# Kernel optimization log

Measured on AMD Instinct MI355X. Metric: run time of the kernel, lower is better.

## Reference

```python
import jax, jax.numpy as jnp
import numpy as np

N = 100000
E = 3200000
F_IN = 512
HID = 8
NC = 64


def setup_inputs() -> dict:
    key = jax.random.key(0)
    ks = jax.random.split(key, 12)
    x = jax.random.normal(ks[0], (N, F_IN), dtype=jnp.float32)
    edge_index = jax.random.randint(ks[1], (2, E), 0, N, dtype=jnp.int64)
    # layer 1: lin(512 -> 8), wmlp: Linear(1,8,no bias) -> LeakyReLU(0.2) -> Linear(8,8,bias)
    W1 = jax.random.normal(ks[2], (F_IN, HID), dtype=jnp.float32) / np.sqrt(F_IN)
    b1 = jnp.zeros((HID,), dtype=jnp.float32)
    mW1a = jax.random.normal(ks[3], (1, HID), dtype=jnp.float32)
    mW1b = jax.random.normal(ks[4], (HID, HID), dtype=jnp.float32) / np.sqrt(HID)
    mb1 = jnp.zeros((HID,), dtype=jnp.float32)
    # layer 2: lin(8 -> 64), wmlp: Linear(1,64,no bias) -> LeakyReLU(0.2) -> Linear(64,64,bias)
    W2 = jax.random.normal(ks[5], (HID, NC), dtype=jnp.float32) / np.sqrt(HID)
    b2 = jnp.zeros((NC,), dtype=jnp.float32)
    mW2a = jax.random.normal(ks[6], (1, NC), dtype=jnp.float32)
    mW2b = jax.random.normal(ks[7], (NC, NC), dtype=jnp.float32) / np.sqrt(NC)
    mb2 = jnp.zeros((NC,), dtype=jnp.float32)
    return {"x": x, "edge_index": edge_index,
            "W1": W1, "b1": b1, "mW1a": mW1a, "mW1b": mW1b, "mb1": mb1,
            "W2": W2, "b2": b2, "mW2a": mW2a, "mW2b": mW2b, "mb2": mb2}


def _rcgn(x, edge_index, W, b, mWa, mWb, mb):
    n = x.shape[0]
    h = x @ W + b                                   # [N, C]
    row, col = edge_index[0], edge_index[1]
    # degree of source nodes only (matches degree(row, ...))
    deg = jax.ops.segment_sum(jnp.ones_like(row, dtype=h.dtype), row, num_segments=n)
    dinv = jnp.where(deg > 0, deg ** -0.5, 0.0)     # guard isolated nodes
    norm = (dinv[row] * dinv[col])[:, None]          # [E, 1]
    # per-edge MLP on scalar norm -> per-edge per-channel weight [E, C]
    w = jax.nn.leaky_relu(norm @ mWa, 0.2) @ mWb + mb
    msg = w * h[row]                                 # gather + elementwise [E, C]
    return jax.ops.segment_sum(msg, col, num_segments=n)  # scatter-add to targets


def reference(x, edge_index, W1, b1, mW1a, mW1b, mb1, W2, b2, mW2a, mW2b, mb2):
    # eval mode: dropout layers are identity
    h = _rcgn(x, edge_index, W1, b1, mW1a, mW1b, mb1)
    h = jax.nn.elu(h)
    h = _rcgn(h, edge_index, W2, b2, mW2a, mW2b, mb2)
    return jax.nn.log_softmax(h, axis=1)
```

## Files before the change

### kernel.cpp

```cpp
#include <hip/hip_runtime.h>
#include <hip/hip_bf16.h>
#include <math.h>

#define NNODES 100000
#define NEDGES 3200000
#define FIN 512
#define HID 8
#define NC 64

#define OFF_DEG      0u
#define OFF_CNT      1600000u
#define OFF_DINV     3200000u
#define OFF_COLPTR   3600000u
#define OFF_BSUM     4000004u
#define OFF_BOFF     4000516u
#define OFF_A1       4001028u
#define OFF_A2       4001060u
#define OFF_AUX      4001316u
#define OFF_CSR      7201320u
#define OFF_H1       0u
#define OFF_H2       32801320u

__global__ __launch_bounds__(256) void k_count(const int* __restrict__ ei,
                                               int* __restrict__ deg, int* __restrict__ cnt,
                                               unsigned char* __restrict__ aux) {
    int t = blockIdx.x * blockDim.x + threadIdx.x;
    if (t < NEDGES) {
        atomicAdd(&deg[ei[t] << 2], 1);
        int rank = atomicAdd(&cnt[ei[NEDGES + t] << 2], 1);
        aux[t] = (unsigned char)rank;
    }
}

__global__ __launch_bounds__(1024) void k_scan1(const int* __restrict__ cnt,
                                                const int* __restrict__ deg,
                                                float* __restrict__ dinv,
                                                int* __restrict__ colptr, int* __restrict__ bsum) {
    __shared__ int s[1024];
    int t = threadIdx.x, b = blockIdx.x;
    int i = b * 1024 + t;
    int v = (i < NNODES) ? cnt[i << 2] : 0;
    if (i < NNODES) {
        int d = deg[i << 2];
        dinv[i] = (d > 0) ? 1.0f / sqrtf((float)d) : 0.0f;
    }
    s[t] = v; __syncthreads();
    for (int off = 1; off < 1024; off <<= 1) {
        int add = (t >= off) ? s[t - off] : 0;
        __syncthreads();
        s[t] += add;
        __syncthreads();
    }
    if (i < NNODES) colptr[i + 1] = s[t];
    if (t == 1023) bsum[b] = s[1023];
}

__global__ __launch_bounds__(128) void k_scan2(const int* __restrict__ bsum,
                                               int* __restrict__ boff, int nb) {
    __shared__ int s[128];
    int t = threadIdx.x;
    int v = (t < nb) ? bsum[t] : 0;
    s[t] = v; __syncthreads();
    for (int off = 1; off < 128; off <<= 1) {
        int add = (t >= off) ? s[t - off] : 0;
        __syncthreads();
        s[t] += add;
        __syncthreads();
    }
    if (t < nb) boff[t] = s[t] - v;
}

__global__ __launch_bounds__(1024) void k_scan3(int* __restrict__ colptr, const int* __restrict__ boff) {
    int i = blockIdx.x * blockDim.x + threadIdx.x;
    if (i < NNODES) colptr[i + 1] += boff[i >> 10];
    if (i == 0) colptr[0] = 0;
}

__global__ __launch_bounds__(64) void k_precomp(const float* __restrict__ mW1a, const float* __restrict__ mW1b,
                                                const float* __restrict__ mW2a, const float* __restrict__ mW2b,
                                                float* __restrict__ A1, float* __restrict__ A2) {
    int t = threadIdx.x;
    if (t < 8) {
        float s = 0.f;
        for (int j = 0; j < 8; j++) {
            float a = mW1a[j]; a = a > 0.f ? a : 0.2f * a;
            s += a * mW1b[j * 8 + t];
        }
        A1[t] = s;
    }
    if (t < 64) {
        float s = 0.f;
        for (int j = 0; j < 64; j++) {
            float a = mW2a[j]; a = a > 0.f ? a : 0.2f * a;
            s += a * mW2b[j * 64 + t];
        }
        A2[t] = s;
    }
}

__global__ __launch_bounds__(256) void k_fill(const int* __restrict__ ei, const float* __restrict__ dinv,
                                              const int* __restrict__ colptr,
                                              const unsigned char* __restrict__ aux,
                                              int2* __restrict__ csr) {
    int t = blockIdx.x * blockDim.x + threadIdx.x;
    if (t < NEDGES) {
        int r = ei[t], c = ei[NEDGES + t];
        float nm = dinv[r] * dinv[c];
        int pos = colptr[c] + (int)aux[t];
        csr[pos] = make_int2(r, __float_as_int(nm));
    }
}

__global__ __launch_bounds__(256) void k_gemm1(const float* __restrict__ x, const float* __restrict__ W1,
                                               const float* __restrict__ b1, float* __restrict__ h1) {
    __shared__ float w[HID * FIN];
    for (int idx = threadIdx.x; idx < HID * FIN; idx += 256) {
        int j = idx >> 3, k = idx & 7;
        w[k * FIN + j] = W1[idx];
    }
    __syncthreads();
    int lane = threadIdx.x & 63;
    int node = blockIdx.x * 4 + (threadIdx.x >> 6);
    const float* xr = x + (size_t)node * FIN;
    float acc[8] = {0.f,0.f,0.f,0.f,0.f,0.f,0.f,0.f};
#pragma unroll
    for (int tt = 0; tt < 8; tt++) {
        float xv = xr[lane + 64 * tt];
#pragma unroll
        for (int k = 0; k < 8; k++)
            acc[k] += xv * w[k * FIN + lane + 64 * tt];
    }
    {
        bool hi = (lane & 32) != 0;
#pragma unroll
        for (int m = 0; m < 4; m++) {
            float send = hi ? acc[m] : acc[m + 4];
            float recv = __shfl_xor(send, 32, 64);
            acc[m] = (hi ? acc[m + 4] : acc[m]) + recv;
        }
    }
    {
        bool hi = (lane & 16) != 0;
#pragma unroll
        for (int m = 0; m < 2; m++) {
            float send = hi ? acc[m] : acc[m + 2];
            float recv = __shfl_xor(send, 16, 64);
            acc[m] = (hi ? acc[m + 2] : acc[m]) + recv;
        }
    }
    {
        bool hi = (lane & 8) != 0;
        float send = hi ? acc[0] : acc[1];
        float recv = __shfl_xor(send, 8, 64);
        acc[0] = (hi ? acc[1] : acc[0]) + recv;
    }
    acc[0] += __shfl_xor(acc[0], 4, 64);
    acc[0] += __shfl_xor(acc[0], 2, 64);
    acc[0] += __shfl_xor(acc[0], 1, 64);
    if ((lane & 7) == 0) {
        int k = (lane >> 3) & 7;
        h1[(size_t)node * HID + k] = acc[0] + b1[k];
    }
}

__global__ __launch_bounds__(256) void k_agg1(const int* __restrict__ colptr, const int2* __restrict__ csr,
                                              const float* __restrict__ h1, const float* __restrict__ A1,
                                              const float* __restrict__ mb1, const float* __restrict__ W2,
                                              const float* __restrict__ b2, float* __restrict__ h2) {
    int lane = threadIdx.x & 63;
    int node = blockIdx.x * 4 + (threadIdx.x >> 6);
    int k = lane & 7, esub = lane >> 3;
    float a1 = A1[k], m1 = mb1[k];
    int s = colptr[node], e = colptr[node + 1];
    float acc = 0.f;
    for (int i = s + esub; i < e; i += 8) {
        int2 ed = csr[i];
        float nm = __int_as_float(ed.y);
        acc += (nm * a1 + m1) * h1[(size_t)ed.x * HID + k];
    }
    acc += __shfl_xor(acc, 8, 64);
    acc += __shfl_xor(acc, 16, 64);
    acc += __shfl_xor(acc, 32, 64);
    float hv = acc > 0.f ? acc : expm1f(acc);
    float o = b2[lane];
#pragma unroll
    for (int j = 0; j < 8; j++) {
        float ev = __shfl(hv, j, 64);
        o += ev * W2[j * NC + lane];
    }
    h2[(size_t)node * NC + lane] = o;
}

__global__ __launch_bounds__(256) void k_agg2(const int* __restrict__ colptr, const int2* __restrict__ csr,
                                              const float* __restrict__ h2, const float* __restrict__ A2,
                                              const float* __restrict__ mb2, float* __restrict__ out) {
    int lane = threadIdx.x & 63;
    int node = blockIdx.x * 4 + (threadIdx.x >> 6);
    float a2 = A2[lane], m2 = mb2[lane];
    int s = colptr[node], e = colptr[node + 1];
    float acc = 0.f;
    int i = s;
    for (; i + 4 <= e; i += 4) {
        int2 e0 = csr[i], e1 = csr[i + 1], e2 = csr[i + 2], e3 = csr[i + 3];
        float h0 = h2[(size_t)e0.x * NC + lane];
        float h1v = h2[(size_t)e1.x * NC + lane];
        float h2v = h2[(size_t)e2.x * NC + lane];
        float h3 = h2[(size_t)e3.x * NC + lane];
        acc += (__int_as_float(e0.y) * a2 + m2) * h0;
        acc += (__int_as_float(e1.y) * a2 + m2) * h1v;
        acc += (__int_as_float(e2.y) * a2 + m2) * h2v;
        acc += (__int_as_float(e3.y) * a2 + m2) * h3;
    }
    for (; i < e; i++) {
        int2 ed = csr[i];
        acc += (__int_as_float(ed.y) * a2 + m2) * h2[(size_t)ed.x * NC + lane];
    }
    float m = acc;
#pragma unroll
    for (int o = 32; o >= 1; o >>= 1) m = fmaxf(m, __shfl_xor(m, o, 64));
    float ex = expf(acc - m);
    float ssum = ex;
#pragma unroll
    for (int o = 32; o >= 1; o >>= 1) ssum += __shfl_xor(ssum, o, 64);
    out[(size_t)node * NC + lane] = (acc - m) - logf(ssum);
}

extern "C" void kernel_launch(void* const* d_in, const int* in_sizes, int n_in,
                              void* d_out, int out_size, void* d_ws, size_t ws_size,
                              hipStream_t stream) {
    const float* x    = (const float*)d_in[0];
    const int*   ei   = (const int*)d_in[1];
    const float* W1   = (const float*)d_in[2];
    const float* b1   = (const float*)d_in[3];
    const float* mW1a = (const float*)d_in[4];
    const float* mW1b = (const float*)d_in[5];
    const float* mb1  = (const float*)d_in[6];
    const float* W2   = (const float*)d_in[7];
    const float* b2   = (const float*)d_in[8];
    const float* mW2a = (const float*)d_in[9];
    const float* mW2b = (const float*)d_in[10];
    const float* mb2  = (const float*)d_in[11];

    char* ws = (char*)d_ws;
    int*   deg    = (int*)(ws + OFF_DEG);
    int*   cnt    = (int*)(ws + OFF_CNT);
    float* dinv   = (float*)(ws + OFF_DINV);
    int*   colptr = (int*)(ws + OFF_COLPTR);
    int*   bsum   = (int*)(ws + OFF_BSUM);
    int*   boff   = (int*)(ws + OFF_BOFF);
    float* A1     = (float*)(ws + OFF_A1);
    float* A2     = (float*)(ws + OFF_A2);
    unsigned char* aux = (unsigned char*)(ws + OFF_AUX);
    int2*  csr    = (int2*)(ws + OFF_CSR);
    float* h1     = (float*)(ws + OFF_H1);
    float* h2     = (float*)(ws + OFF_H2);
    float* outp   = (float*)d_out;

    hipMemsetAsync(ws, 0, 3200000, stream);

    const int EB = (NEDGES + 255) / 256;
    const int SB = (NNODES + 1023) / 1024;

    k_count  <<<EB, 256, 0, stream>>>(ei, deg, cnt, aux);
    k_scan1  <<<SB, 1024, 0, stream>>>(cnt, deg, dinv, colptr, bsum);
    k_scan2  <<<1, 128, 0, stream>>>(bsum, boff, SB);
    k_scan3  <<<SB, 1024, 0, stream>>>(colptr, boff);
    k_precomp<<<1, 64, 0, stream>>>(mW1a, mW1b, mW2a, mW2b, A1, A2);
    k_fill   <<<EB, 256, 0, stream>>>(ei, dinv, colptr, aux, csr);
    k_gemm1  <<<NNODES / 4, 256, 0, stream>>>(x, W1, b1, h1);
    k_agg1   <<<NNODES / 4, 256, 0, stream>>>(colptr, csr, h1, A1, mb1, W2, b2, h2);
    k_agg2   <<<NNODES / 4, 256, 0, stream>>>(colptr, csr, h2, A2, mb2, outp);
}
```

Measured before the change: 880.1 us.

## Compute source degrees via LDS-privatized range histograms; register-resident W1 in gemm1

Replaces the global atomic degree count with a two-pass scheme. Blocks build shared-memory histograms over node-range/edge-chunk tiles into a slab, then a reduce kernel sums the slabs and writes dinv. The target-count atomics drop their 4x padding stride, and the workspace layout and memset shrink. The first GEMM now loads W1 rows into registers with float4 loads and reads x as float4 instead of staging W1 transposed in shared memory. The histogram pass reads the row array 8 times, and each thread now holds 64 weight registers.

```diff
diff --git a/kernel.cpp b/kernel.cpp
--- a/kernel.cpp
+++ b/kernel.cpp
@@ -8,42 +8,67 @@
 #define HID 8
 #define NC 64
 
-#define OFF_DEG      0u
-#define OFF_CNT      1600000u
-#define OFF_DINV     3200000u
-#define OFF_COLPTR   3600000u
-#define OFF_BSUM     4000004u
-#define OFF_BOFF     4000516u
-#define OFF_A1       4001028u
-#define OFF_A2       4001060u
-#define OFF_AUX      4001316u
-#define OFF_CSR      7201320u
-#define OFF_H1       0u
-#define OFF_H2       32801320u
+#define NRANGE 8
+#define NCHUNK 32
+#define ECHUNK (NEDGES / NCHUNK)
+#define RBINS  12500
+#define RPAD   12512
+
+#define OFF_CNT      0u
+#define OFF_DINV     400000u
+#define OFF_COLPTR   800000u
+#define OFF_BSUM     1200004u
+#define OFF_BOFF     1200516u
+#define OFF_A1       1201028u
+#define OFF_A2       1201060u
+#define OFF_AUX      1201316u
+#define OFF_H1       1201316u
+#define OFF_CSR      4401320u
+#define OFF_H2       30001320u
+
+__global__ __launch_bounds__(1024) void k_hist(const int* __restrict__ ei, int* __restrict__ slab) {
+    __shared__ int lh[RBINS];
+    int ri = blockIdx.x & 7, ci = blockIdx.x >> 3;
+    for (int b = threadIdx.x; b < RBINS; b += 1024) lh[b] = 0;
+    __syncthreads();
+    int base = ri * RBINS;
+    const int* rows = ei + (size_t)ci * ECHUNK;
+    for (int t = threadIdx.x; t < ECHUNK; t += 1024) {
+        int r = rows[t] - base;
+        if ((unsigned)r < RBINS) atomicAdd(&lh[r], 1);
+    }
+    __syncthreads();
+    int* out = slab + (size_t)blockIdx.x * RPAD;
+    for (int b = threadIdx.x; b < RBINS; b += 1024) out[b] = lh[b];
+}
+
+__global__ __launch_bounds__(256) void k_reduce(const int* __restrict__ slab, float* __restrict__ dinv) {
+    int i = blockIdx.x * 256 + threadIdx.x;
+    if (i >= NNODES) return;
+    int ri = i / RBINS, b = i - ri * RBINS;
+    int s = 0;
+#pragma unroll 4
+    for (int ci = 0; ci < NCHUNK; ci++)
+        s += slab[(size_t)(ci * NRANGE + ri) * RPAD + b];
+    dinv[i] = (s > 0) ? 1.0f / sqrtf((float)s) : 0.0f;
+}
 
 __global__ __launch_bounds__(256) void k_count(const int* __restrict__ ei,
-                                               int* __restrict__ deg, int* __restrict__ cnt,
+                                               int* __restrict__ cnt,
                                                unsigned char* __restrict__ aux) {
     int t = blockIdx.x * blockDim.x + threadIdx.x;
     if (t < NEDGES) {
-        atomicAdd(&deg[ei[t] << 2], 1);
-        int rank = atomicAdd(&cnt[ei[NEDGES + t] << 2], 1);
+        int rank = atomicAdd(&cnt[ei[NEDGES + t]], 1);
         aux[t] = (unsigned char)rank;
     }
 }
 
 __global__ __launch_bounds__(1024) void k_scan1(const int* __restrict__ cnt,
-                                                const int* __restrict__ deg,
-                                                float* __restrict__ dinv,
                                                 int* __restrict__ colptr, int* __restrict__ bsum) {
     __shared__ int s[1024];
     int t = threadIdx.x, b = blockIdx.x;
     int i = b * 1024 + t;
-    int v = (i < NNODES) ? cnt[i << 2] : 0;
-    if (i < NNODES) {
-        int d = deg[i << 2];
-        dinv[i] = (d > 0) ? 1.0f / sqrtf((float)d) : 0.0f;
-    }
+    int v = (i < NNODES) ? cnt[i] : 0;
     s[t] = v; __syncthreads();
     for (int off = 1; off < 1024; off <<= 1) {
         int add = (t >= off) ? s[t - off] : 0;
@@ -113,22 +138,32 @@
 
 __global__ __launch_bounds__(256) void k_gemm1(const float* __restrict__ x, const float* __restrict__ W1,
                                                const float* __restrict__ b1, float* __restrict__ h1) {
-    __shared__ float w[HID * FIN];
-    for (int idx = threadIdx.x; idx < HID * FIN; idx += 256) {
-        int j = idx >> 3, k = idx & 7;
-        w[k * FIN + j] = W1[idx];
-    }
-    __syncthreads();
     int lane = threadIdx.x & 63;
     int node = blockIdx.x * 4 + (threadIdx.x >> 6);
-    const float* xr = x + (size_t)node * FIN;
+    float w[8][8];
+#pragma unroll
+    for (int tf = 0; tf < 2; tf++) {
+        int jf = lane + 64 * tf;
+#pragma unroll
+        for (int m = 0; m < 4; m++) {
+            const float4* Wr = (const float4*)(W1 + (size_t)(4 * jf + m) * 8);
+            float4 lo = Wr[0], hi = Wr[1];
+            int r = 4 * tf + m;
+            w[r][0] = lo.x; w[r][1] = lo.y; w[r][2] = lo.z; w[r][3] = lo.w;
+            w[r][4] = hi.x; w[r][5] = hi.y; w[r][6] = hi.z; w[r][7] = hi.w;
+        }
+    }
+    const float4* xr = (const float4*)(x + (size_t)node * FIN);
     float acc[8] = {0.f,0.f,0.f,0.f,0.f,0.f,0.f,0.f};
 #pragma unroll
-    for (int tt = 0; tt < 8; tt++) {
-        float xv = xr[lane + 64 * tt];
-#pragma unroll
-        for (int k = 0; k < 8; k++)
-            acc[k] += xv * w[k * FIN + lane + 64 * tt];
+    for (int tf = 0; tf < 2; tf++) {
+        float4 xv = xr[lane + 64 * tf];
+        float xs[4] = {xv.x, xv.y, xv.z, xv.w};
+#pragma unroll
+        for (int m = 0; m < 4; m++)
+#pragma unroll
+            for (int k = 0; k < 8; k++)
+                acc[k] += xs[m] * w[4 * tf + m][k];
     }
     {
         bool hi = (lane & 32) != 0;
@@ -242,7 +277,6 @@
     const float* mb2  = (const float*)d_in[11];
 
     char* ws = (char*)d_ws;
-    int*   deg    = (int*)(ws + OFF_DEG);
     int*   cnt    = (int*)(ws + OFF_CNT);
     float* dinv   = (float*)(ws + OFF_DINV);
     int*   colptr = (int*)(ws + OFF_COLPTR);
@@ -251,18 +285,21 @@
     float* A1     = (float*)(ws + OFF_A1);
     float* A2     = (float*)(ws + OFF_A2);
     unsigned char* aux = (unsigned char*)(ws + OFF_AUX);
+    int*   slab   = (int*)(ws + OFF_CSR);
     int2*  csr    = (int2*)(ws + OFF_CSR);
     float* h1     = (float*)(ws + OFF_H1);
     float* h2     = (float*)(ws + OFF_H2);
     float* outp   = (float*)d_out;
 
-    hipMemsetAsync(ws, 0, 3200000, stream);
+    hipMemsetAsync(ws, 0, 400000, stream);
 
     const int EB = (NEDGES + 255) / 256;
     const int SB = (NNODES + 1023) / 1024;
 
-    k_count  <<<EB, 256, 0, stream>>>(ei, deg, cnt, aux);
-    k_scan1  <<<SB, 1024, 0, stream>>>(cnt, deg, dinv, colptr, bsum);
+    k_hist   <<<NRANGE * NCHUNK, 1024, 0, stream>>>(ei, slab);
+    k_reduce <<<(NNODES + 255) / 256, 256, 0, stream>>>(slab, dinv);
+    k_count  <<<EB, 256, 0, stream>>>(ei, cnt, aux);
+    k_scan1  <<<SB, 1024, 0, stream>>>(cnt, colptr, bsum);
     k_scan2  <<<1, 128, 0, stream>>>(bsum, boff, SB);
     k_scan3  <<<SB, 1024, 0, stream>>>(colptr, boff);
     k_precomp<<<1, 64, 0, stream>>>(mW1a, mW1b, mW2a, mW2b, A1, A2);
```

Result: no change. 865.5 us (-1.6%).
